# Kernel tuning notes

Hardware: AMD Instinct MI355X
Metric: run time of the kernel (lower is better)

## Reference

```python
import jax, jax.numpy as jnp
import numpy as np

_A1 = jnp.array([[1.,0.,0.,0.],[0.,1.,0.,0.],[0.,0.,1.,0.],[0.,0.,0.,1.]], dtype=jnp.float32)
_AI = jnp.array([[0.,-1.,0.,0.],[1.,0.,0.,0.],[0.,0.,0.,-1.],[0.,0.,1.,0.]], dtype=jnp.float32)
_AJ = jnp.array([[0.,0.,-1.,0.],[0.,0.,0.,1.],[1.,0.,0.,0.],[0.,-1.,0.,0.]], dtype=jnp.float32)
_AK = jnp.array([[0.,0.,0.,-1.],[0.,0.,-1.,0.],[0.,1.,0.,0.],[1.,0.,0.,0.]], dtype=jnp.float32)

IN_FEATURES = 1024
OUT_FEATURES = 1024
Q_IN = IN_FEATURES // 4
Q_OUT = OUT_FEATURES // 4

def _xavier_uniform(key, shape, gain=0.5):
    fan_out, fan_in = shape
    limit = gain * float(np.sqrt(6.0 / (fan_in + fan_out)))
    return jax.random.uniform(key, shape, jnp.float32, -limit, limit)

def setup_inputs() -> dict:
    key = jax.random.key(0)
    kx, kr, ki, kj, kk = jax.random.split(key, 5)
    x = jax.random.normal(kx, (8, 4096, IN_FEATURES), dtype=jnp.float32)
    R = _xavier_uniform(kr, (Q_OUT, Q_IN))
    I = _xavier_uniform(ki, (Q_OUT, Q_IN))
    J = _xavier_uniform(kj, (Q_OUT, Q_IN))
    K = _xavier_uniform(kk, (Q_OUT, Q_IN))
    bias = jnp.zeros((OUT_FEATURES,), dtype=jnp.float32)
    return {"x": x, "R": R, "I": I, "J": J, "K": K, "bias": bias}

def _build_weight(R, I, J, K):
    # W = kron(A1,R) + kron(AI,I) + kron(AJ,J) + kron(AK,K), shape (4*q_out, 4*q_in)
    # Assemble as 4x4 signed block grid in one einsum-style broadcast.
    # blocks[a,b] = A1[a,b]*R + AI[a,b]*I + AJ[a,b]*J + AK[a,b]*K
    blocks = (_A1[:, :, None, None] * R + _AI[:, :, None, None] * I
              + _AJ[:, :, None, None] * J + _AK[:, :, None, None] * K)  # [4,4,qo,qi]
    qo, qi = R.shape
    return blocks.transpose(0, 2, 1, 3).reshape(4 * qo, 4 * qi)

def reference(x, R, I, J, K, bias):
    W = _build_weight(R, I, J, K)
    return jnp.einsum('bsi,oi->bso', x, W) + bias
```

## Files before the change

### kernel.cpp

```cpp
#include <hip/hip_runtime.h>
#include <hip/hip_bf16.h>

typedef __attribute__((ext_vector_type(4))) float f32x4;
typedef __attribute__((ext_vector_type(4))) uint u32x4;
typedef __attribute__((ext_vector_type(8))) short bf16x8;

#define M_TOTAL 32768
#define N_TOTAL 1024
#define K_TOTAL 1024

__device__ __forceinline__ uint pk2(float a, float b) {
  __hip_bfloat162 h = __float22bfloat162_rn(make_float2(a, b));
  uint u;
  __builtin_memcpy(&u, &h, 4);
  return u;
}

#define SOFT_BARRIER() do {                                                   \
    __builtin_amdgcn_sched_barrier(0);                                        \
    asm volatile("s_waitcnt lgkmcnt(0)" ::: "memory");                        \
    __builtin_amdgcn_s_barrier();                                             \
    __builtin_amdgcn_sched_barrier(0);                                        \
  } while (0)

__global__ __launch_bounds__(256) void conv_x(
    const float* __restrict__ X, ushort* __restrict__ wsx)
{
  const int g = blockIdx.x * 256 + (int)threadIdx.x;
  const int wid = g >> 6;
  const int lane = g & 63;
  const int fm = wid >> 5;
  const int kb = wid & 31;
  const float* p = X + (size_t)(fm * 16 + (lane & 15)) * K_TOTAL
                     + kb * 32 + (lane >> 4) * 8;
  f32x4 lo = *(const f32x4*)p;
  f32x4 hi = *(const f32x4*)(p + 4);
  u32x4 v;
  v[0] = pk2(lo[0], lo[1]); v[1] = pk2(lo[2], lo[3]);
  v[2] = pk2(hi[0], hi[1]); v[3] = pk2(hi[2], hi[3]);
  *(u32x4*)(wsx + (size_t)wid * 512 + lane * 8) = v;
}

__global__ __launch_bounds__(256) void conv_b(
    const float* __restrict__ Rm, const float* __restrict__ Im,
    const float* __restrict__ Jm, const float* __restrict__ Km,
    ushort* __restrict__ ws)
{
  const int slot = blockIdx.x * 256 + (int)threadIdx.x;
  const int lane = slot & 63;
  const int kb = (slot >> 6) & 7;
  const int cb = (slot >> 9) & 15;
  const int si = slot >> 13;
  const float* S = (si == 0) ? Rm : (si == 1) ? Im : (si == 2) ? Jm : Km;
  const float* p = S + (cb * 16 + (lane & 15)) * 256 + kb * 32 + (lane >> 4) * 8;
  f32x4 lo = *(const f32x4*)p;
  f32x4 hi = *(const f32x4*)(p + 4);
  u32x4 v;
  v[0] = pk2(lo[0], lo[1]); v[1] = pk2(lo[2], lo[3]);
  v[2] = pk2(hi[0], hi[1]); v[3] = pk2(hi[2], hi[3]);
  *(u32x4*)(ws + (size_t)slot * 8) = v;
}

#define LOADF(kk, AF, BF) do {                                                \
    const int kbf0_ = (kk) >> 5;                                              \
    _Pragma("unroll")                                                         \
    for (int mi = 0; mi < 4; ++mi)                                            \
      _Pragma("unroll")                                                       \
      for (int ks = 0; ks < 2; ++ks)                                          \
        AF[mi * 2 + ks] = *(const bf16x8*)(                                   \
            WSX + (size_t)((fm0 + mi) * 32 + kbf0_ + ks) * 512 + lane * 8);   \
    const int si_ = a_idx ^ ((kk) >> 8);                                      \
    const int kbq_ = ((kk) & 255) >> 5;                                       \
    _Pragma("unroll")                                                         \
    for (int ks = 0; ks < 2; ++ks)                                            \
      _Pragma("unroll")                                                       \
      for (int ni = 0; ni < 4; ++ni)                                          \
        BF[ks * 4 + ni] = *(const bf16x8*)(                                   \
            WSB + (size_t)((si_ * 16 + cb0 + ni) * 8 + kbq_ + ks) * 512       \
            + lane * 8);                                                      \
  } while (0)

#define SGNFIX(kk, BF) do {                                                   \
    if ((0x284Eu >> ((a_idx << 2) | ((kk) >> 8))) & 1u) {                     \
      _Pragma("unroll")                                                       \
      for (int f = 0; f < 8; ++f) {                                           \
        u32x4 u_ = __builtin_bit_cast(u32x4, BF[f]);                          \
        u_[0] ^= 0x80008000u; u_[1] ^= 0x80008000u;                           \
        u_[2] ^= 0x80008000u; u_[3] ^= 0x80008000u;                           \
        BF[f] = __builtin_bit_cast(bf16x8, u_);                               \
      }                                                                       \
    }                                                                         \
  } while (0)

#define MFMAS(AF, BF) do {                                                    \
    _Pragma("unroll")                                                         \
    for (int ks = 0; ks < 2; ++ks)                                            \
      _Pragma("unroll")                                                       \
      for (int mi = 0; mi < 4; ++mi)                                          \
        _Pragma("unroll")                                                     \
        for (int ni = 0; ni < 4; ++ni)                                        \
          acc[mi][ni] = __builtin_amdgcn_mfma_f32_16x16x32_bf16(              \
              AF[mi * 2 + ks], BF[ks * 4 + ni], acc[mi][ni], 0, 0, 0);        \
  } while (0)

__global__ __launch_bounds__(256, 2) void qlin_gemm5(
    const ushort* __restrict__ WSX, const ushort* __restrict__ WSB,
    const float* __restrict__ bias, float* __restrict__ Y)
{
  const int per = 2048 >> 3;
  const int bid = (int)blockIdx.x;
  const int swz = (bid & 7) * per + (bid >> 3);
  const int mblk = swz >> 2;
  const int a_idx = swz & 3;
  const int n0 = a_idx << 8;
  const int m0 = mblk << 6;
  const int fm0 = mblk << 2;

  const int tid = (int)threadIdx.x;
  const int lane = tid & 63;
  const int w = tid >> 6;
  const int cb0 = w << 2;

  bf16x8 A0[8], B0[8], A1[8], B1[8];
  f32x4 acc[4][4];
#pragma unroll
  for (int i = 0; i < 4; ++i)
#pragma unroll
    for (int j = 0; j < 4; ++j) acc[i][j] = (f32x4)(0.0f);

  LOADF(0, A0, B0);
#pragma unroll 1
  for (int k = 0; k < 16; k += 2) {
    const int kk0 = k << 6;
    if (k + 1 < 16) LOADF(kk0 + 64, A1, B1);
    SGNFIX(kk0, B0);
    MFMAS(A0, B0);
    if (k + 2 < 16) LOADF(kk0 + 128, A0, B0);
    SGNFIX(kk0 + 64, B1);
    MFMAS(A1, B1);
  }

#pragma unroll
  for (int ni = 0; ni < 4; ++ni) {
    const int col = n0 + (w << 6) + (ni << 4) + (lane & 15);
    const float bv = bias[col];
#pragma unroll
    for (int mi = 0; mi < 4; ++mi) {
      const int r0e = m0 + (mi << 4) + ((lane >> 4) << 2);
#pragma unroll
      for (int j = 0; j < 4; ++j)
        Y[(size_t)(r0e + j) * N_TOTAL + col] = acc[mi][ni][j] + bv;
    }
  }
}

#define BM2 256
#define BN2 256
#define BK2 64
#define NT2 512
#define NSTEPS2 (K_TOTAL / BK2)

#define LOAD_A2(kk) do {                                                      \
    _Pragma("unroll")                                                         \
    for (int cc = 0; cc < 4; ++cc) {                                          \
      const float* pa_ = X + (size_t)(m0 + r0 + 64 * cc) * K_TOTAL + (kk) + k0;\
      rA[2 * cc]     = *(const f32x4*)pa_;                                    \
      rA[2 * cc + 1] = *(const f32x4*)(pa_ + 4);                              \
    }                                                                         \
  } while (0)

#define COMMIT_A2(dst) do {                                                   \
    _Pragma("unroll")                                                         \
    for (int cc = 0; cc < 4; ++cc) {                                          \
      u32x4 va_;                                                              \
      va_[0] = pk2(rA[2 * cc][0], rA[2 * cc][1]);                             \
      va_[1] = pk2(rA[2 * cc][2], rA[2 * cc][3]);                             \
      va_[2] = pk2(rA[2 * cc + 1][0], rA[2 * cc + 1][1]);                     \
      va_[3] = pk2(rA[2 * cc + 1][2], rA[2 * cc + 1][3]);                     \
      *(u32x4*)((dst) + sbase + 8192 * cc) = va_;                             \
    }                                                                         \
  } while (0)

#define LOAD_B2(kk) do {                                                      \
    const int bsel_ = (kk) >> 8;                                              \
    const int si_ = a_idx ^ bsel_;                                            \
    const int kbq_ = ((kk) & 255) >> 5;                                       \
    const ushort* fb_ = WS + ((size_t)((si_ * 16 + wc4) * 8 + kbq_)) * 512    \
                        + lane * 8;                                           \
    _Pragma("unroll")                                                         \
    for (int ks = 0; ks < 2; ++ks)                                            \
      _Pragma("unroll")                                                       \
      for (int ni = 0; ni < 4; ++ni)                                          \
        bq[ks * 4 + ni] = *(const bf16x8*)(fb_ + (ni * 8 + ks) * 512);        \
    if ((0x284Eu >> ((a_idx << 2) | bsel_)) & 1u) {                           \
      _Pragma("unroll")                                                       \
      for (int f = 0; f < 8; ++f) {                                           \
        u32x4 u_ = __builtin_bit_cast(u32x4, bq[f]);                          \
        u_[0] ^= 0x80008000u; u_[1] ^= 0x80008000u;                           \
        u_[2] ^= 0x80008000u; u_[3] ^= 0x80008000u;                           \
        bq[f] = __builtin_bit_cast(bf16x8, u_);                               \
      }                                                                       \
    }                                                                         \
  } while (0)

#define COMPUTE2(src) do {                                                    \
    _Pragma("unroll")                                                         \
    for (int ks = 0; ks < 2; ++ks) {                                          \
      _Pragma("unroll")                                                       \
      for (int mi = 0; mi < 8; ++mi) {                                        \
        const int row_ = frow_a0 + (mi << 4);                                 \
        const int kb_ = (ks << 6) + fkb;                                      \
        bf16x8 af_ = *(const bf16x8*)((src) + row_ * (BK2 * 2)                \
                                      + (kb_ ^ ((row_ & 7) << 4)));           \
        _Pragma("unroll")                                                     \
        for (int ni = 0; ni < 4; ++ni)                                        \
          acc[mi][ni] = __builtin_amdgcn_mfma_f32_16x16x32_bf16(              \
              af_, bq[ks * 4 + ni], acc[mi][ni], 0, 0, 0);                    \
      }                                                                       \
    }                                                                         \
  } while (0)

__global__ __launch_bounds__(NT2, 2) void qlin_gemm2(
    const float* __restrict__ X, const ushort* __restrict__ WS,
    const float* __restrict__ bias, float* __restrict__ Y)
{
  const int per = ((M_TOTAL / BM2) * (N_TOTAL / BN2)) >> 3;
  const int bid = (int)blockIdx.x;
  const int swz = (bid & 7) * per + (bid >> 3);
  const int m0 = (swz >> 2) * BM2;
  const int nblk = swz & 3;
  const int n0 = nblk * BN2;
  const int a_idx = nblk;

  const int tid = (int)threadIdx.x;
  const int lane = tid & 63;
  const int wave = tid >> 6;
  const int wm = (wave >> 2) << 7;
  const int wc4 = (wave & 3) << 2;

  __shared__ __align__(16) ushort smA[2 * BM2 * BK2];
  char* const cS = (char*)smA;

  const int r0 = tid >> 3;
  const int k0 = (tid & 7) << 3;
  const int sbase = r0 * (BK2 * 2) + ((k0 * 2) ^ ((r0 & 7) << 4));

  f32x4 rA[8];
  bf16x8 bq[8];
  f32x4 acc[8][4];
#pragma unroll
  for (int i = 0; i < 8; ++i)
#pragma unroll
    for (int j = 0; j < 4; ++j) acc[i][j] = (f32x4)(0.0f);

  const int frow_a0 = wm + (lane & 15);
  const int fkb = (lane >> 4) << 4;

  LOAD_A2(0);
  COMMIT_A2(cS);
  LOAD_A2(BK2);
  SOFT_BARRIER();

#pragma unroll 1
  for (int k = 0; k < NSTEPS2; ++k) {
    char* const rbuf = cS + ((k & 1) << 15);
    char* const wbuf = cS + (((k + 1) & 1) << 15);
    COMMIT_A2(wbuf);
    LOAD_B2(k * BK2);
    if (k + 2 < NSTEPS2) LOAD_A2((k + 2) * BK2);
    COMPUTE2(rbuf);
    SOFT_BARRIER();
  }

#pragma unroll
  for (int ni = 0; ni < 4; ++ni) {
    const int col = n0 + (wc4 << 4) + (ni << 4) + (lane & 15);
    const float bv = bias[col];
#pragma unroll
    for (int mi = 0; mi < 8; ++mi) {
      const int r0e = m0 + wm + (mi << 4) + ((lane >> 4) << 2);
#pragma unroll
      for (int j = 0; j < 4; ++j)
        Y[(size_t)(r0e + j) * N_TOTAL + col] = acc[mi][ni][j] + bv;
    }
  }
}

#define BM 128
#define BN 128
#define BK 64
#define NTHREADS 256
#define NSTEPS (K_TOTAL / BK)

#define LOAD_TILE(kk) do {                                                    \
    const int si_ = a_idx ^ ((kk) >> 8);                                      \
    const float* Bsrc_ = (si_ == 0) ? Rm : (si_ == 1) ? Im                    \
                       : (si_ == 2) ? Jm : Km;                                \
    const int kloc_ = (kk) & 255;                                             \
    _Pragma("unroll")                                                         \
    for (int cc = 0; cc < 4; ++cc) {                                          \
      const float* pa_ = X + (size_t)(m0 + r0 + 32 * cc) * K_TOTAL + (kk) + k0;\
      rA[2 * cc]     = *(const f32x4*)pa_;                                    \
      rA[2 * cc + 1] = *(const f32x4*)(pa_ + 4);                              \
      const float* pb_ = Bsrc_ + (o_src + r0 + 32 * cc) * 256 + kloc_ + k0;   \
      rB[2 * cc]     = *(const f32x4*)pb_;                                    \
      rB[2 * cc + 1] = *(const f32x4*)(pb_ + 4);                              \
    }                                                                         \
  } while (0)

#define COMMIT_TILE(kk, dst) do {                                             \
    const uint neg_ = (0x284Eu >> ((a_idx << 2) | ((kk) >> 8))) & 1u;         \
    _Pragma("unroll")                                                         \
    for (int cc = 0; cc < 4; ++cc) {                                          \
      u32x4 va_;                                                              \
      va_[0] = pk2(rA[2 * cc][0], rA[2 * cc][1]);                             \
      va_[1] = pk2(rA[2 * cc][2], rA[2 * cc][3]);                             \
      va_[2] = pk2(rA[2 * cc + 1][0], rA[2 * cc + 1][1]);                     \
      va_[3] = pk2(rA[2 * cc + 1][2], rA[2 * cc + 1][3]);                     \
      *(u32x4*)((dst) + sbase + 4096 * cc) = va_;                             \
    }                                                                         \
    if (neg_) {                                                               \
      _Pragma("unroll")                                                       \
      for (int cc = 0; cc < 4; ++cc) {                                        \
        u32x4 vb_;                                                            \
        vb_[0] = pk2(-rB[2 * cc][0], -rB[2 * cc][1]);                         \
        vb_[1] = pk2(-rB[2 * cc][2], -rB[2 * cc][3]);                         \
        vb_[2] = pk2(-rB[2 * cc + 1][0], -rB[2 * cc + 1][1]);                 \
        vb_[3] = pk2(-rB[2 * cc + 1][2], -rB[2 * cc + 1][3]);                 \
        *(u32x4*)((dst) + 16384 + sbase + 4096 * cc) = vb_;                   \
      }                                                                       \
    } else {                                                                  \
      _Pragma("unroll")                                                       \
      for (int cc = 0; cc < 4; ++cc) {                                        \
        u32x4 vb_;                                                            \
        vb_[0] = pk2(rB[2 * cc][0], rB[2 * cc][1]);                           \
        vb_[1] = pk2(rB[2 * cc][2], rB[2 * cc][3]);                           \
        vb_[2] = pk2(rB[2 * cc + 1][0], rB[2 * cc + 1][1]);                   \
        vb_[3] = pk2(rB[2 * cc + 1][2], rB[2 * cc + 1][3]);                   \
        *(u32x4*)((dst) + 16384 + sbase + 4096 * cc) = vb_;                   \
      }                                                                       \
    }                                                                         \
  } while (0)

#define COMPUTE_TILE(src) do {                                                \
    _Pragma("unroll")                                                         \
    for (int ks = 0; ks < 2; ++ks) {                                          \
      const int kb_ = (ks << 6) + fkb;                                        \
      bf16x8 af_[4], bf_[4];                                                  \
      _Pragma("unroll")                                                       \
      for (int mi = 0; mi < 4; ++mi) {                                        \
        const int row_ = frow_a0 + (mi << 4);                                 \
        af_[mi] = *(const bf16x8*)((src) + row_ * (BK * 2)                    \
                                   + (kb_ ^ ((row_ & 7) << 4)));              \
      }                                                                       \
      _Pragma("unroll")                                                       \
      for (int ni = 0; ni < 4; ++ni) {                                        \
        const int row_ = frow_b0 + (ni << 4);                                 \
        bf_[ni] = *(const bf16x8*)((src) + 16384 + row_ * (BK * 2)            \
                                   + (kb_ ^ ((row_ & 7) << 4)));              \
      }                                                                       \
      _Pragma("unroll")                                                       \
      for (int mi = 0; mi < 4; ++mi)                                          \
        _Pragma("unroll")                                                     \
        for (int ni = 0; ni < 4; ++ni)                                        \
          acc[mi][ni] = __builtin_amdgcn_mfma_f32_16x16x32_bf16(              \
              af_[mi], bf_[ni], acc[mi][ni], 0, 0, 0);                        \
    }                                                                         \
  } while (0)

__global__ __launch_bounds__(NTHREADS, 2) void qlin_gemm(
    const float* __restrict__ X, const float* __restrict__ Rm,
    const float* __restrict__ Im, const float* __restrict__ Jm,
    const float* __restrict__ Km, const float* __restrict__ bias,
    float* __restrict__ Y)
{
  const int per = ((M_TOTAL / BM) * (N_TOTAL / BN)) >> 3;
  const int bid = (int)blockIdx.x;
  const int swz = (bid & 7) * per + (bid >> 3);
  const int m0 = (swz >> 3) * BM;
  const int n0 = (swz & 7) * BN;

  const int tid = (int)threadIdx.x;
  const int lane = tid & 63;
  const int wave = tid >> 6;
  const int wm = (wave >> 1) << 6;
  const int wn = (wave & 1) << 6;

  __shared__ __align__(16) ushort sm[2 * 2 * BM * BK];
  char* const cS = (char*)sm;

  const int a_idx = n0 >> 8;
  const int o_src = n0 & 255;

  const int r0 = tid >> 3;
  const int k0 = (tid & 7) << 3;
  const int sbase = r0 * (BK * 2) + ((k0 * 2) ^ ((r0 & 7) << 4));

  f32x4 rA[8], rB[8];
  f32x4 acc[4][4];
#pragma unroll
  for (int i = 0; i < 4; ++i)
#pragma unroll
    for (int j = 0; j < 4; ++j) acc[i][j] = (f32x4)(0.0f);

  const int frow_a0 = wm + (lane & 15);
  const int frow_b0 = wn + (lane & 15);
  const int fkb = (lane >> 4) << 4;

  LOAD_TILE(0);
  COMMIT_TILE(0, cS);
  LOAD_TILE(BK);
  SOFT_BARRIER();

#pragma unroll 1
  for (int k = 0; k < NSTEPS; ++k) {
    char* const rbuf = cS + ((k & 1) << 15);
    char* const wbuf = cS + (((k + 1) & 1) << 15);
    if (k + 1 < NSTEPS) COMMIT_TILE((k + 1) * BK, wbuf);
    if (k + 2 < NSTEPS) LOAD_TILE((k + 2) * BK);
    COMPUTE_TILE(rbuf);
    SOFT_BARRIER();
  }

#pragma unroll
  for (int ni = 0; ni < 4; ++ni) {
    const int col = n0 + wn + (ni << 4) + (lane & 15);
    const float bv = bias[col];
#pragma unroll
    for (int mi = 0; mi < 4; ++mi) {
      const int r0e = m0 + wm + (mi << 4) + ((lane >> 4) << 2);
#pragma unroll
      for (int j = 0; j < 4; ++j)
        Y[(size_t)(r0e + j) * N_TOTAL + col] = acc[mi][ni][j] + bv;
    }
  }
}

extern "C" void kernel_launch(void* const* d_in, const int* in_sizes, int n_in,
                              void* d_out, int out_size, void* d_ws, size_t ws_size,
                              hipStream_t stream) {
  const float* X = (const float*)d_in[0];
  const float* Rm = (const float*)d_in[1];
  const float* Im = (const float*)d_in[2];
  const float* Jm = (const float*)d_in[3];
  const float* Km = (const float*)d_in[4];
  const float* bias = (const float*)d_in[5];
  float* Y = (float*)d_out;

  const size_t needB = (size_t)4 * 256 * 256 * 2;
  const size_t needX = (size_t)M_TOTAL * K_TOTAL * 2;

  if (ws_size >= needX + needB) {
    ushort* wsx = (ushort*)d_ws;
    ushort* wsb = wsx + (size_t)M_TOTAL * K_TOTAL;
    conv_x<<<dim3(16384), dim3(256), 0, stream>>>(X, wsx);
    conv_b<<<dim3(128), dim3(256), 0, stream>>>(Rm, Im, Jm, Km, wsb);
    qlin_gemm5<<<dim3(2048), dim3(256), 0, stream>>>(wsx, wsb, bias, Y);
  } else if (ws_size >= needB) {
    ushort* wsb = (ushort*)d_ws;
    conv_b<<<dim3(128), dim3(256), 0, stream>>>(Rm, Im, Jm, Km, wsb);
    qlin_gemm2<<<dim3((M_TOTAL / BM2) * (N_TOTAL / BN2)), dim3(NT2), 0, stream>>>(
        X, wsb, bias, Y);
  } else {
    qlin_gemm<<<dim3((M_TOTAL / BM) * (N_TOTAL / BN)), dim3(NTHREADS), 0, stream>>>(
        X, Rm, Im, Jm, Km, bias, Y);
  }
}
```

Baseline: 131.6 us.

## Stage X tiles in LDS via direct global-to-LDS loads with larger 256x256 blocks

Replaces the register-only 64x256 GEMM with a 512-thread, 256x256-tile kernel. Each A tile is staged into double-buffered LDS using global_load_lds and shared across four waves. B fragments stay in registers. This cuts redundant global reads of X and raises reuse per block, at the cost of a full vmcnt wait plus a barrier each k-step, more accumulator registers (8x4 per wave), and fewer blocks (512).

```diff
diff --git a/kernel.cpp b/kernel.cpp
--- a/kernel.cpp
+++ b/kernel.cpp
@@ -19,6 +19,13 @@
 #define SOFT_BARRIER() do {                                                   \
     __builtin_amdgcn_sched_barrier(0);                                        \
     asm volatile("s_waitcnt lgkmcnt(0)" ::: "memory");                        \
+    __builtin_amdgcn_s_barrier();                                             \
+    __builtin_amdgcn_sched_barrier(0);                                        \
+  } while (0)
+
+#define WAITV0_BAR() do {                                                     \
+    __builtin_amdgcn_sched_barrier(0);                                        \
+    asm volatile("s_waitcnt vmcnt(0) lgkmcnt(0)" ::: "memory");               \
     __builtin_amdgcn_s_barrier();                                             \
     __builtin_amdgcn_sched_barrier(0);                                        \
   } while (0)
@@ -61,27 +68,34 @@
   *(u32x4*)(ws + (size_t)slot * 8) = v;
 }
 
-#define LOADF(kk, AF, BF) do {                                                \
-    const int kbf0_ = (kk) >> 5;                                              \
-    _Pragma("unroll")                                                         \
-    for (int mi = 0; mi < 4; ++mi)                                            \
-      _Pragma("unroll")                                                       \
-      for (int ks = 0; ks < 2; ++ks)                                          \
-        AF[mi * 2 + ks] = *(const bf16x8*)(                                   \
-            WSX + (size_t)((fm0 + mi) * 32 + kbf0_ + ks) * 512 + lane * 8);   \
-    const int si_ = a_idx ^ ((kk) >> 8);                                      \
-    const int kbq_ = ((kk) & 255) >> 5;                                       \
+#define NT6 512
+
+#define STAGE6(kt, dst) do {                                                  \
+    _Pragma("unroll")                                                         \
+    for (int j = 0; j < 4; ++j) {                                             \
+      const int f_ = (wv << 2) + j;                                           \
+      const ushort* s_ = WSX                                                  \
+          + ((size_t)(fmB + (f_ >> 1)) * 32 + (kt) * 2 + (f_ & 1)) * 512      \
+          + lane * 8;                                                         \
+      __builtin_amdgcn_global_load_lds((const uint*)s_,                       \
+                                       (uint*)((dst) + f_ * 512), 16, 0, 0);  \
+    }                                                                         \
+  } while (0)
+
+#define LOADB6(kt, BF) do {                                                   \
+    const int si_ = a_idx ^ ((kt) >> 2);                                      \
+    const int kbq_ = ((kt) & 3) << 1;                                         \
     _Pragma("unroll")                                                         \
     for (int ks = 0; ks < 2; ++ks)                                            \
       _Pragma("unroll")                                                       \
       for (int ni = 0; ni < 4; ++ni)                                          \
         BF[ks * 4 + ni] = *(const bf16x8*)(                                   \
-            WSB + (size_t)((si_ * 16 + cb0 + ni) * 8 + kbq_ + ks) * 512       \
+            WSB + ((size_t)((si_ * 16 + cb0 + ni) * 8 + kbq_ + ks)) * 512     \
             + lane * 8);                                                      \
   } while (0)
 
-#define SGNFIX(kk, BF) do {                                                   \
-    if ((0x284Eu >> ((a_idx << 2) | ((kk) >> 8))) & 1u) {                     \
+#define SGN6(kt, BF) do {                                                     \
+    if ((0x284Eu >> ((a_idx << 2) | ((kt) >> 2))) & 1u) {                     \
       _Pragma("unroll")                                                       \
       for (int f = 0; f < 8; ++f) {                                           \
         u32x4 u_ = __builtin_bit_cast(u32x4, BF[f]);                          \
@@ -92,61 +106,76 @@
     }                                                                         \
   } while (0)
 
-#define MFMAS(AF, BF) do {                                                    \
-    _Pragma("unroll")                                                         \
-    for (int ks = 0; ks < 2; ++ks)                                            \
-      _Pragma("unroll")                                                       \
-      for (int mi = 0; mi < 4; ++mi)                                          \
+#define COMPUTE6(src, BF) do {                                                \
+    _Pragma("unroll")                                                         \
+    for (int ks = 0; ks < 2; ++ks) {                                          \
+      _Pragma("unroll")                                                       \
+      for (int mi = 0; mi < 8; ++mi) {                                        \
+        bf16x8 af_ = *(const bf16x8*)((src)                                   \
+            + ((fmW + mi) * 2 + ks) * 512 + lane * 8);                        \
         _Pragma("unroll")                                                     \
         for (int ni = 0; ni < 4; ++ni)                                        \
           acc[mi][ni] = __builtin_amdgcn_mfma_f32_16x16x32_bf16(              \
-              AF[mi * 2 + ks], BF[ks * 4 + ni], acc[mi][ni], 0, 0, 0);        \
-  } while (0)
-
-__global__ __launch_bounds__(256, 2) void qlin_gemm5(
+              af_, BF[ks * 4 + ni], acc[mi][ni], 0, 0, 0);                    \
+      }                                                                       \
+    }                                                                         \
+  } while (0)
+
+__global__ __launch_bounds__(NT6, 2) void qlin_gemm6(
     const ushort* __restrict__ WSX, const ushort* __restrict__ WSB,
     const float* __restrict__ bias, float* __restrict__ Y)
 {
-  const int per = 2048 >> 3;
+  const int per = 512 >> 3;
   const int bid = (int)blockIdx.x;
   const int swz = (bid & 7) * per + (bid >> 3);
-  const int mblk = swz >> 2;
+  const int mb = swz >> 2;
   const int a_idx = swz & 3;
   const int n0 = a_idx << 8;
-  const int m0 = mblk << 6;
-  const int fm0 = mblk << 2;
+  const int m0 = mb << 8;
+  const int fmB = mb << 4;
 
   const int tid = (int)threadIdx.x;
   const int lane = tid & 63;
-  const int w = tid >> 6;
-  const int cb0 = w << 2;
-
-  bf16x8 A0[8], B0[8], A1[8], B1[8];
-  f32x4 acc[4][4];
-#pragma unroll
-  for (int i = 0; i < 4; ++i)
+  const int wv = tid >> 6;
+  const int fmW = (wv >> 2) << 3;
+  const int cb0 = (wv & 3) << 2;
+  const int wm = (wv >> 2) << 7;
+  const int wn = (wv & 3) << 6;
+
+  __shared__ __align__(16) ushort smA[2 * 256 * 64];
+  ushort* const buf0 = smA;
+  ushort* const buf1 = smA + 256 * 64;
+
+  bf16x8 bq0[8], bq1[8];
+  f32x4 acc[8][4];
+#pragma unroll
+  for (int i = 0; i < 8; ++i)
 #pragma unroll
     for (int j = 0; j < 4; ++j) acc[i][j] = (f32x4)(0.0f);
 
-  LOADF(0, A0, B0);
+  STAGE6(0, buf0);
+  LOADB6(0, bq0);
+
 #pragma unroll 1
   for (int k = 0; k < 16; k += 2) {
-    const int kk0 = k << 6;
-    if (k + 1 < 16) LOADF(kk0 + 64, A1, B1);
-    SGNFIX(kk0, B0);
-    MFMAS(A0, B0);
-    if (k + 2 < 16) LOADF(kk0 + 128, A0, B0);
-    SGNFIX(kk0 + 64, B1);
-    MFMAS(A1, B1);
+    WAITV0_BAR();
+    STAGE6(k + 1, buf1);
+    LOADB6(k + 1, bq1);
+    SGN6(k, bq0);
+    COMPUTE6(buf0, bq0);
+    WAITV0_BAR();
+    if (k + 2 < 16) { STAGE6(k + 2, buf0); LOADB6(k + 2, bq0); }
+    SGN6(k + 1, bq1);
+    COMPUTE6(buf1, bq1);
   }
 
 #pragma unroll
   for (int ni = 0; ni < 4; ++ni) {
-    const int col = n0 + (w << 6) + (ni << 4) + (lane & 15);
+    const int col = n0 + wn + (ni << 4) + (lane & 15);
     const float bv = bias[col];
 #pragma unroll
-    for (int mi = 0; mi < 4; ++mi) {
-      const int r0e = m0 + (mi << 4) + ((lane >> 4) << 2);
+    for (int mi = 0; mi < 8; ++mi) {
+      const int r0e = m0 + wm + (mi << 4) + ((lane >> 4) << 2);
 #pragma unroll
       for (int j = 0; j < 4; ++j)
         Y[(size_t)(r0e + j) * N_TOTAL + col] = acc[mi][ni][j] + bv;
@@ -455,7 +484,7 @@
     ushort* wsb = wsx + (size_t)M_TOTAL * K_TOTAL;
     conv_x<<<dim3(16384), dim3(256), 0, stream>>>(X, wsx);
     conv_b<<<dim3(128), dim3(256), 0, stream>>>(Rm, Im, Jm, Km, wsb);
-    qlin_gemm5<<<dim3(2048), dim3(256), 0, stream>>>(wsx, wsb, bias, Y);
+    qlin_gemm6<<<dim3(512), dim3(NT6), 0, stream>>>(wsx, wsb, bias, Y);
   } else if (ws_size >= needB) {
     ushort* wsb = (ushort*)d_ws;
     conv_b<<<dim3(128), dim3(256), 0, stream>>>(Rm, Im, Jm, Km, wsb);
```

Result: slower. 190.1 us (+44.4%).

## Switch direct-load GEMM to 128x128 block tiles with 2x2 warp grid

Applied to the files above, without the earlier changes.

Replaces the 64x256 block tile (four waves each owning 64x64 along N) with a 128x128 tile split as a 2x2 wave grid. The K step per stage drops from 64 to 32, halving the fragment registers held per stage, and launch bounds rise from 2 to 3 blocks per SIMD group to raise occupancy. The square tile means each block fetches the same total of A and B fragments from global memory as before, but rebalanced between A and B. The cost is twice as many loop iterations and less latency hiding per stage.

```diff
diff --git a/kernel.cpp b/kernel.cpp
--- a/kernel.cpp
+++ b/kernel.cpp
@@ -61,29 +61,27 @@
   *(u32x4*)(ws + (size_t)slot * 8) = v;
 }
 
-#define LOADF(kk, AF, BF) do {                                                \
-    const int kbf0_ = (kk) >> 5;                                              \
+#define LOADA7(s, AF) do {                                                    \
     _Pragma("unroll")                                                         \
     for (int mi = 0; mi < 4; ++mi)                                            \
-      _Pragma("unroll")                                                       \
-      for (int ks = 0; ks < 2; ++ks)                                          \
-        AF[mi * 2 + ks] = *(const bf16x8*)(                                   \
-            WSX + (size_t)((fm0 + mi) * 32 + kbf0_ + ks) * 512 + lane * 8);   \
-    const int si_ = a_idx ^ ((kk) >> 8);                                      \
-    const int kbq_ = ((kk) & 255) >> 5;                                       \
-    _Pragma("unroll")                                                         \
-    for (int ks = 0; ks < 2; ++ks)                                            \
-      _Pragma("unroll")                                                       \
-      for (int ni = 0; ni < 4; ++ni)                                          \
-        BF[ks * 4 + ni] = *(const bf16x8*)(                                   \
-            WSB + (size_t)((si_ * 16 + cb0 + ni) * 8 + kbq_ + ks) * 512       \
-            + lane * 8);                                                      \
-  } while (0)
-
-#define SGNFIX(kk, BF) do {                                                   \
-    if ((0x284Eu >> ((a_idx << 2) | ((kk) >> 8))) & 1u) {                     \
-      _Pragma("unroll")                                                       \
-      for (int f = 0; f < 8; ++f) {                                           \
+      AF[mi] = *(const bf16x8*)(                                              \
+          WSX + ((size_t)(fmA + mi) * 32 + (s)) * 512 + lane * 8);            \
+  } while (0)
+
+#define LOADB7(s, BF) do {                                                    \
+    const int si_ = a_idx ^ ((s) >> 3);                                       \
+    const int kbq_ = (s) & 7;                                                 \
+    _Pragma("unroll")                                                         \
+    for (int ni = 0; ni < 4; ++ni)                                            \
+      BF[ni] = *(const bf16x8*)(                                              \
+          WSB + ((size_t)((si_ * 16 + cb0 + ni) * 8 + kbq_)) * 512            \
+          + lane * 8);                                                        \
+  } while (0)
+
+#define SGN7(s, BF) do {                                                      \
+    if ((0x284Eu >> ((a_idx << 2) | ((s) >> 3))) & 1u) {                      \
+      _Pragma("unroll")                                                       \
+      for (int f = 0; f < 4; ++f) {                                           \
         u32x4 u_ = __builtin_bit_cast(u32x4, BF[f]);                          \
         u_[0] ^= 0x80008000u; u_[1] ^= 0x80008000u;                           \
         u_[2] ^= 0x80008000u; u_[3] ^= 0x80008000u;                           \
@@ -92,61 +90,63 @@
     }                                                                         \
   } while (0)
 
-#define MFMAS(AF, BF) do {                                                    \
-    _Pragma("unroll")                                                         \
-    for (int ks = 0; ks < 2; ++ks)                                            \
-      _Pragma("unroll")                                                       \
-      for (int mi = 0; mi < 4; ++mi)                                          \
-        _Pragma("unroll")                                                     \
-        for (int ni = 0; ni < 4; ++ni)                                        \
-          acc[mi][ni] = __builtin_amdgcn_mfma_f32_16x16x32_bf16(              \
-              AF[mi * 2 + ks], BF[ks * 4 + ni], acc[mi][ni], 0, 0, 0);        \
-  } while (0)
-
-__global__ __launch_bounds__(256, 2) void qlin_gemm5(
+#define MFMA7(AF, BF) do {                                                    \
+    _Pragma("unroll")                                                         \
+    for (int mi = 0; mi < 4; ++mi)                                            \
+      _Pragma("unroll")                                                       \
+      for (int ni = 0; ni < 4; ++ni)                                          \
+        acc[mi][ni] = __builtin_amdgcn_mfma_f32_16x16x32_bf16(                \
+            AF[mi], BF[ni], acc[mi][ni], 0, 0, 0);                            \
+  } while (0)
+
+__global__ __launch_bounds__(256, 3) void qlin_gemm7(
     const ushort* __restrict__ WSX, const ushort* __restrict__ WSB,
     const float* __restrict__ bias, float* __restrict__ Y)
 {
   const int per = 2048 >> 3;
   const int bid = (int)blockIdx.x;
   const int swz = (bid & 7) * per + (bid >> 3);
-  const int mblk = swz >> 2;
-  const int a_idx = swz & 3;
-  const int n0 = a_idx << 8;
-  const int m0 = mblk << 6;
-  const int fm0 = mblk << 2;
+  const int mblk = swz >> 3;
+  const int nblk = swz & 7;
+  const int m0 = mblk << 7;
+  const int n0 = nblk << 7;
+  const int a_idx = nblk >> 1;
 
   const int tid = (int)threadIdx.x;
   const int lane = tid & 63;
-  const int w = tid >> 6;
-  const int cb0 = w << 2;
-
-  bf16x8 A0[8], B0[8], A1[8], B1[8];
+  const int wv = tid >> 6;
+  const int wr = wv >> 1;
+  const int wc = wv & 1;
+  const int fmA = (mblk << 3) + (wr << 2);
+  const int cb0 = ((nblk & 1) << 3) + (wc << 2);
+
+  bf16x8 a0[4], b0[4], a1[4], b1[4];
   f32x4 acc[4][4];
 #pragma unroll
   for (int i = 0; i < 4; ++i)
 #pragma unroll
     for (int j = 0; j < 4; ++j) acc[i][j] = (f32x4)(0.0f);
 
-  LOADF(0, A0, B0);
+  LOADA7(0, a0);
+  LOADB7(0, b0);
+
 #pragma unroll 1
-  for (int k = 0; k < 16; k += 2) {
-    const int kk0 = k << 6;
-    if (k + 1 < 16) LOADF(kk0 + 64, A1, B1);
-    SGNFIX(kk0, B0);
-    MFMAS(A0, B0);
-    if (k + 2 < 16) LOADF(kk0 + 128, A0, B0);
-    SGNFIX(kk0 + 64, B1);
-    MFMAS(A1, B1);
+  for (int s = 0; s < 32; s += 2) {
+    if (s + 1 < 32) { LOADA7(s + 1, a1); LOADB7(s + 1, b1); }
+    SGN7(s, b0);
+    MFMA7(a0, b0);
+    if (s + 2 < 32) { LOADA7(s + 2, a0); LOADB7(s + 2, b0); }
+    SGN7(s + 1, b1);
+    MFMA7(a1, b1);
   }
 
 #pragma unroll
   for (int ni = 0; ni < 4; ++ni) {
-    const int col = n0 + (w << 6) + (ni << 4) + (lane & 15);
+    const int col = n0 + (wc << 6) + (ni << 4) + (lane & 15);
     const float bv = bias[col];
 #pragma unroll
     for (int mi = 0; mi < 4; ++mi) {
-      const int r0e = m0 + (mi << 4) + ((lane >> 4) << 2);
+      const int r0e = m0 + (wr << 6) + (mi << 4) + ((lane >> 4) << 2);
 #pragma unroll
       for (int j = 0; j < 4; ++j)
         Y[(size_t)(r0e + j) * N_TOTAL + col] = acc[mi][ni][j] + bv;
@@ -455,7 +455,7 @@
     ushort* wsb = wsx + (size_t)M_TOTAL * K_TOTAL;
     conv_x<<<dim3(16384), dim3(256), 0, stream>>>(X, wsx);
     conv_b<<<dim3(128), dim3(256), 0, stream>>>(Rm, Im, Jm, Km, wsb);
-    qlin_gemm5<<<dim3(2048), dim3(256), 0, stream>>>(wsx, wsb, bias, Y);
+    qlin_gemm7<<<dim3(2048), dim3(256), 0, stream>>>(wsx, wsb, bias, Y);
   } else if (ws_size >= needB) {
     ushort* wsb = (ushort*)d_ws;
     conv_b<<<dim3(128), dim3(256), 0, stream>>>(Rm, Im, Jm, Km, wsb);
```

After: 126.4 us. 4.0% less time.
